# Kernel optimization log

Hardware: AMD Instinct MI355X
Metric: run time of the kernel (lower is better)

Reference implementation:

```python
import jax, jax.numpy as jnp
import numpy as np
import math

B, C, N = 8, 128, 16384
H = 4
DK = C // H
COUT = 128
EPS = 1e-5

def _ln(x, g, b):
    # x: (B,H,N,DK); g,b: (H,DK) -> per-head LayerNorm over last dim
    mu = jnp.mean(x, axis=-1, keepdims=True)
    var = jnp.mean((x - mu) ** 2, axis=-1, keepdims=True)
    xh = (x - mu) / jnp.sqrt(var + EPS)
    return xh * g[None, :, None, :] + b[None, :, None, :]

def setup_inputs() -> dict:
    key = jax.random.key(0)
    ks = jax.random.split(key, 12)
    s = 0.02
    return {
        "x": jax.random.normal(ks[0], (B, C, N), jnp.float32),
        "Wq": jax.random.normal(ks[1], (C, C), jnp.float32) * s + 0.01 * jnp.eye(C),
        "bq": jnp.zeros((C,), jnp.float32),
        "Wk": jax.random.normal(ks[2], (C, C), jnp.float32) * s + 0.01 * jnp.eye(C),
        "bk": jnp.zeros((C,), jnp.float32),
        "Wv": jax.random.normal(ks[3], (C, C), jnp.float32) * s + 0.01 * jnp.eye(C),
        "bv": jnp.zeros((C,), jnp.float32),
        "gK": jnp.ones((H, DK), jnp.float32),
        "bK": jnp.zeros((H, DK), jnp.float32),
        "gV": jnp.ones((H, DK), jnp.float32),
        "bV": jnp.zeros((H, DK), jnp.float32),
        "Wo": jax.random.normal(ks[4], (COUT, C), jnp.float32) * s,
        "bo": jnp.zeros((COUT,), jnp.float32),
    }

def reference(x, Wq, bq, Wk, bk, Wv, bv, gK, bK, gV, bV, Wo, bo):
    # x: (B, C, N) -> (B, N, C)
    xt = jnp.transpose(x, (0, 2, 1))
    def proj(W, b):
        y = xt @ W.T + b                      # (B,N,C)
        return jnp.transpose(y.reshape(B, N, H, DK), (0, 2, 1, 3))  # (B,H,N,DK)
    q = proj(Wq, bq)
    k = proj(Wk, bk)
    v = proj(Wv, bv)
    # galerkin: per-head LayerNorm on K and V (vectorized over heads)
    k = _ln(k, gK, bK)
    v = _ln(v, gV, bV)
    # linear (no-softmax) attention: (Q K^T / sqrt(dk)) / N @ V == Q @ (K^T V) / (sqrt(dk)*N)
    # dropout from F.dropout is treated as identity (deterministic reference)
    kv = jnp.einsum("bhnd,bhne->bhde", k, v)            # (B,H,DK,DK)
    attn = jnp.einsum("bhnd,bhde->bhne", q, kv) / (math.sqrt(DK) * N)
    out = jnp.transpose(attn, (0, 2, 1, 3)).reshape(B, N, C)  # merge heads
    out = out @ Wo.T + bo                                # (B,N,COUT)
    return jnp.transpose(out, (0, 2, 1))                 # (B,COUT,N)
```

## Files before the change

### kernel.cpp

```cpp
#include <hip/hip_runtime.h>
#include <cmath>

#define BB 8
#define CC 128
#define NN 16384
#define HH 4
#define NBK 64
#define SX 272

typedef __attribute__((ext_vector_type(8))) short bf16x8;
typedef __attribute__((ext_vector_type(4))) float f32x4;

#define MFMA(a, b, c) __builtin_amdgcn_mfma_f32_16x16x32_bf16(a, b, c, 0, 0, 0)

__device__ __forceinline__ unsigned short f2b(float f) {
  union { float f; unsigned u; } v; v.f = f;
  unsigned r = v.u + 0x7FFFu + ((v.u >> 16) & 1u);
  return (unsigned short)(r >> 16);
}

__device__ __forceinline__ int xt_addr(int n, int cblk) {
  return n * SX + ((cblk ^ ((n >> 2) & 7)) << 4);
}
__device__ __forceinline__ int kt_byte(int c, int n) {
  return c * 144 + ((((n >> 3) ^ (c & 7)) << 4) | ((n & 7) << 1));
}

__global__ void k_prep(const float* __restrict__ Wq, const float* __restrict__ Wk,
                       const float* __restrict__ Wv, const float* __restrict__ Wo,
                       unsigned short* __restrict__ Wb) {
  const int idx = blockIdx.x * 256 + threadIdx.x;
  const int which = idx >> 14;
  const float* src = (which == 0) ? Wq : (which == 1) ? Wk : (which == 2) ? Wv : Wo;
  Wb[idx] = f2b(src[idx & 16383]);
}

__global__ __launch_bounds__(1024)
void k_xpose(const float* __restrict__ x, unsigned char* __restrict__ xTg) {
  extern __shared__ char lds[];
  const int tid = threadIdx.x;
  const int lane = tid & 63;
  const int w = tid >> 6;
  const int b = blockIdx.y;
  const int n0 = blockIdx.x * 512;

#pragma unroll
  for (int seg = 0; seg < 2; ++seg) {
    const float* xb = x + ((size_t)b * CC + w * 8) * NN + n0 + seg * 256 + lane * 4;
    f32x4 va[8];
#pragma unroll
    for (int cc = 0; cc < 8; ++cc) va[cc] = *(const f32x4*)(xb + (size_t)cc * NN);
#pragma unroll
    for (int j = 0; j < 4; ++j) {
      const int n = seg * 256 + lane * 4 + j;
      bf16x8 pk;
#pragma unroll
      for (int cc = 0; cc < 8; ++cc)
        ((unsigned short*)&pk)[cc] = f2b(va[cc][j]);
      *(bf16x8*)(lds + n * SX + ((w ^ ((n >> 2) & 7)) << 4)) = pk;
    }
  }
  __syncthreads();
  unsigned char* dst = xTg + ((size_t)b * NN + n0) * SX;
  for (int off = tid * 16; off < 512 * SX; off += 16384)
    *(float4*)(dst + off) = *(const float4*)(lds + off);
}

__global__ __launch_bounds__(512, 4)
void k_fuse1(const unsigned char* __restrict__ xTg,
             const unsigned short* __restrict__ Wkb, const unsigned short* __restrict__ Wvb,
             const float* __restrict__ bk, const float* __restrict__ bv,
             const float* __restrict__ gK, const float* __restrict__ bK,
             const float* __restrict__ gV, const float* __restrict__ bV,
             float* __restrict__ kvp) {
  extern __shared__ char lds[];
  char* XT = lds;
  char* KT = lds + 34816;
  char* VT = lds + 53248;
  float* KVS = (float*)lds;

  const int tid = threadIdx.x;
  const int lane = tid & 63;
  const int w = tid >> 6;
  const int b = blockIdx.y;
  const int bx = blockIdx.x;
  const int l15 = lane & 15, l4 = lane >> 4;

  const int ph = w >> 1, pp = w & 1;
  const int kh = w >> 1, khalf = w & 1;

  const unsigned short* Wsrc = pp ? Wvb : Wkb;
  bf16x8 wf[2][4];
#pragma unroll
  for (int mf = 0; mf < 2; ++mf)
#pragma unroll
    for (int ks = 0; ks < 4; ++ks)
      wf[mf][ks] = *(const bf16x8*)(Wsrc + (ph * 32 + mf * 16 + l15) * 128 + ks * 32 + l4 * 8);

  float bias[2][4], gam[2][4], bet[2][4];
  {
    const float* bsrc = pp ? bv : bk;
    const float* gsrc = pp ? gV : gK;
    const float* esrc = pp ? bV : bK;
#pragma unroll
    for (int mf = 0; mf < 2; ++mf)
#pragma unroll
      for (int r = 0; r < 4; ++r) {
        const int cg = ph * 32 + mf * 16 + l4 * 4 + r;
        bias[mf][r] = bsrc[cg]; gam[mf][r] = gsrc[cg]; bet[mf][r] = esrc[cg];
      }
  }

  f32x4 kvacc[2][2];
#pragma unroll
  for (int i = 0; i < 2; ++i)
#pragma unroll
    for (int j = 0; j < 2; ++j) kvacc[i][j] = (f32x4){0.f, 0.f, 0.f, 0.f};

  for (int ot = 0; ot < 2; ++ot) {
    const int n0 = (bx * 2 + ot) * 128;

    {
      const unsigned char* src = xTg + ((size_t)b * NN + n0) * SX;
      for (int off = tid * 16; off < 128 * SX; off += 8192)
        *(float4*)(XT + off) = *(const float4*)(src + off);
    }
    __syncthreads();

    for (int t = 0; t < 2; ++t) {
      const int nbase = t * 64;
      char* DST = pp ? VT : KT;
#pragma unroll
      for (int nf = 0; nf < 4; ++nf) {
        const int n = nbase + nf * 16 + l15;
        f32x4 a0 = (f32x4){0.f, 0.f, 0.f, 0.f}, a1 = (f32x4){0.f, 0.f, 0.f, 0.f};
#pragma unroll
        for (int ks = 0; ks < 4; ++ks) {
          const bf16x8 xf = *(const bf16x8*)(XT + xt_addr(n, ks * 4 + l4));
          a0 = MFMA(wf[0][ks], xf, a0);
          a1 = MFMA(wf[1][ks], xf, a1);
        }
#pragma unroll
        for (int r = 0; r < 4; ++r) { a0[r] += bias[0][r]; a1[r] += bias[1][r]; }
        float s = 0.f, ss = 0.f;
#pragma unroll
        for (int r = 0; r < 4; ++r) {
          s += a0[r] + a1[r];
          ss += a0[r] * a0[r] + a1[r] * a1[r];
        }
        s += __shfl_xor(s, 16); ss += __shfl_xor(ss, 16);
        s += __shfl_xor(s, 32); ss += __shfl_xor(ss, 32);
        const float mu = s * (1.f / 32.f);
        const float var = ss * (1.f / 32.f) - mu * mu;
        const float rstd = rsqrtf(var + 1e-5f);
        const int nloc = nf * 16 + l15;
#pragma unroll
        for (int r = 0; r < 4; ++r) {
          const int c0k = ph * 32 + l4 * 4 + r;
          *(unsigned short*)(DST + kt_byte(c0k, nloc)) =
              f2b((a0[r] - mu) * rstd * gam[0][r] + bet[0][r]);
          const int c1k = ph * 32 + 16 + l4 * 4 + r;
          *(unsigned short*)(DST + kt_byte(c1k, nloc)) =
              f2b((a1[r] - mu) * rstd * gam[1][r] + bet[1][r]);
        }
      }
      __syncthreads();

#pragma unroll
      for (int mf = 0; mf < 2; ++mf) {
        const int ck = kh * 32 + mf * 16 + l15;
        const bf16x8 ka = *(const bf16x8*)(KT + ck * 144 + (((khalf * 4 + l4) ^ (ck & 7)) << 4));
#pragma unroll
        for (int ef = 0; ef < 2; ++ef) {
          const int cv = kh * 32 + ef * 16 + l15;
          const bf16x8 vb = *(const bf16x8*)(VT + cv * 144 + (((khalf * 4 + l4) ^ (cv & 7)) << 4));
          kvacc[mf][ef] = MFMA(ka, vb, kvacc[mf][ef]);
        }
      }
      __syncthreads();
    }
  }

#pragma unroll
  for (int mf = 0; mf < 2; ++mf)
#pragma unroll
    for (int ef = 0; ef < 2; ++ef)
#pragma unroll
      for (int r = 0; r < 4; ++r) {
        const int d = mf * 16 + l4 * 4 + r, e = ef * 16 + l15;
        KVS[w * 1024 + d * 32 + e] = kvacc[mf][ef][r];
      }
  __syncthreads();
  {
    float* og = kvp + ((size_t)(b * NBK + bx)) * 4096;
#pragma unroll
    for (int i = 0; i < 2; ++i) {
      const int off = i * 2048 + tid * 4;
      const int h = off >> 10, q = off & 1023;
      const f32x4 v0 = *(const f32x4*)(KVS + (2 * h) * 1024 + q);
      const f32x4 v1 = *(const f32x4*)(KVS + (2 * h + 1) * 1024 + q);
      *(f32x4*)(og + off) = v0 + v1;
    }
  }
}

__global__ void k_reduceA(const float* __restrict__ kvp, float* __restrict__ p2) {
  const int blk = blockIdx.x;
  const int s = blk & 7, h = (blk >> 3) & 3, b = blk >> 5;
  const int t = threadIdx.x;
  f32x4 acc = (f32x4){0.f, 0.f, 0.f, 0.f};
  for (int i = 0; i < 8; ++i) {
    const int bx = s * 8 + i;
    acc += *(const f32x4*)(kvp + ((size_t)(b * NBK + bx)) * 4096 + h * 1024 + t * 4);
  }
  *(f32x4*)(p2 + (size_t)blk * 1024 + t * 4) = acc;
}

__global__ void k_reduceB(const float* __restrict__ p2, unsigned short* __restrict__ kvT,
                          const float scale) {
  const int bh = blockIdx.x;
  const int t = threadIdx.x;
  f32x4 acc = (f32x4){0.f, 0.f, 0.f, 0.f};
  for (int s = 0; s < 8; ++s)
    acc += *(const f32x4*)(p2 + ((size_t)bh * 8 + s) * 1024 + t * 4);
#pragma unroll
  for (int j = 0; j < 4; ++j) {
    const int i = t * 4 + j;
    const int d = i >> 5, e = i & 31;
    kvT[(size_t)bh * 1024 + e * 32 + d] = f2b(acc[j] * scale);
  }
}

__global__ __launch_bounds__(512, 4)
void k_pass2(const unsigned char* __restrict__ xTg,
             const unsigned short* __restrict__ Wqb, const float* __restrict__ bq,
             const unsigned short* __restrict__ kvT,
             const unsigned short* __restrict__ Wob, const float* __restrict__ bo,
             float* __restrict__ out) {
  extern __shared__ char lds[];
  char* QS = lds + 34816;
  char* AS = lds + 51200;

  const int tid = threadIdx.x;
  const int lane = tid & 63;
  const int w = tid >> 6;
  const int b = blockIdx.y;
  const int l15 = lane & 15, l4 = lane >> 4;
  const int h = w >> 1, half = w & 1;

  bf16x8 kvf[2];
#pragma unroll
  for (int mf = 0; mf < 2; ++mf)
    kvf[mf] = *(const bf16x8*)(kvT + (((size_t)b * HH + h) * 32 + mf * 16 + l15) * 32 + l4 * 8);
  bf16x8 wq[4], wo[4];
#pragma unroll
  for (int ks = 0; ks < 4; ++ks) {
    wq[ks] = *(const bf16x8*)(Wqb + (w * 16 + l15) * 128 + ks * 32 + l4 * 8);
    wo[ks] = *(const bf16x8*)(Wob + (w * 16 + l15) * 128 + ks * 32 + l4 * 8);
  }
  float bq_r[4], bo_r[4];
#pragma unroll
  for (int r = 0; r < 4; ++r) {
    bq_r[r] = bq[w * 16 + l4 * 4 + r];
    bo_r[r] = bo[w * 16 + l4 * 4 + r];
  }

  float* ob = out + (size_t)b * CC * NN;

  for (int it = 0; it < 4; ++it) {
    const int n0 = blockIdx.x * 256 + it * 64;
    char* XT = (it & 1) ? (lds + 17408) : lds;

    {
      const unsigned char* src = xTg + ((size_t)b * NN + n0) * SX;
      for (int off = tid * 16; off < 64 * SX; off += 8192)
        *(float4*)(XT + off) = *(const float4*)(src + off);
    }
    __syncthreads();

    f32x4 qa[4];
#pragma unroll
    for (int nf = 0; nf < 4; ++nf) qa[nf] = (f32x4){0.f, 0.f, 0.f, 0.f};
#pragma unroll
    for (int ks = 0; ks < 4; ++ks)
#pragma unroll
      for (int nf = 0; nf < 4; ++nf) {
        const int n = nf * 16 + l15;
        const bf16x8 xf = *(const bf16x8*)(XT + xt_addr(n, ks * 4 + l4));
        qa[nf] = MFMA(wq[ks], xf, qa[nf]);
      }
#pragma unroll
    for (int nf = 0; nf < 4; ++nf) {
      const int n = nf * 16 + l15;
      const int c0 = w * 16 + l4 * 4;
      unsigned long long pk = 0;
#pragma unroll
      for (int r = 0; r < 4; ++r)
        pk |= (unsigned long long)f2b(qa[nf][r] + bq_r[r]) << (16 * r);
      *(unsigned long long*)(QS + n * 256 + (((c0 >> 3) ^ (n & 15)) << 4) + ((c0 & 7) << 1)) = pk;
    }
    __syncthreads();

    f32x4 aa[2][2];
#pragma unroll
    for (int i = 0; i < 2; ++i)
#pragma unroll
      for (int j = 0; j < 2; ++j) aa[i][j] = (f32x4){0.f, 0.f, 0.f, 0.f};
    bf16x8 qf[2];
#pragma unroll
    for (int nf = 0; nf < 2; ++nf) {
      const int n = half * 32 + nf * 16 + l15;
      const int cq = h * 32 + l4 * 8;
      qf[nf] = *(const bf16x8*)(QS + n * 256 + ((((cq >> 3)) ^ (n & 15)) << 4));
    }
#pragma unroll
    for (int mf = 0; mf < 2; ++mf)
#pragma unroll
      for (int nf = 0; nf < 2; ++nf) aa[mf][nf] = MFMA(kvf[mf], qf[nf], aa[mf][nf]);
#pragma unroll
    for (int mf = 0; mf < 2; ++mf)
#pragma unroll
      for (int nf = 0; nf < 2; ++nf) {
        const int n = half * 32 + nf * 16 + l15;
        const int e0 = h * 32 + mf * 16 + l4 * 4;
        unsigned long long pk = 0;
#pragma unroll
        for (int r = 0; r < 4; ++r)
          pk |= (unsigned long long)f2b(aa[mf][nf][r]) << (16 * r);
        *(unsigned long long*)(AS + n * 256 + (((e0 >> 3) ^ (n & 15)) << 4) + ((e0 & 7) << 1)) = pk;
      }
    __syncthreads();

    f32x4 oa[4];
#pragma unroll
    for (int nf = 0; nf < 4; ++nf) oa[nf] = (f32x4){0.f, 0.f, 0.f, 0.f};
#pragma unroll
    for (int ks = 0; ks < 4; ++ks)
#pragma unroll
      for (int nf = 0; nf < 4; ++nf) {
        const int n = nf * 16 + l15;
        const bf16x8 af = *(const bf16x8*)(AS + n * 256 + (((ks * 4 + l4) ^ (n & 15)) << 4));
        oa[nf] = MFMA(wo[ks], af, oa[nf]);
      }
#pragma unroll
    for (int nf = 0; nf < 4; ++nf)
#pragma unroll
      for (int r = 0; r < 4; ++r) {
        const int c = w * 16 + l4 * 4 + r;
        ob[(size_t)c * NN + n0 + nf * 16 + l15] = oa[nf][r] + bo_r[r];
      }
  }
}

extern "C" void kernel_launch(void* const* d_in, const int* in_sizes, int n_in,
                              void* d_out, int out_size, void* d_ws, size_t ws_size,
                              hipStream_t stream) {
  const float* x  = (const float*)d_in[0];
  const float* Wq = (const float*)d_in[1];
  const float* bq = (const float*)d_in[2];
  const float* Wk = (const float*)d_in[3];
  const float* bk = (const float*)d_in[4];
  const float* Wv = (const float*)d_in[5];
  const float* bv = (const float*)d_in[6];
  const float* gK = (const float*)d_in[7];
  const float* bK = (const float*)d_in[8];
  const float* gV = (const float*)d_in[9];
  const float* bV = (const float*)d_in[10];
  const float* Wo = (const float*)d_in[11];
  const float* bo = (const float*)d_in[12];
  float* out = (float*)d_out;

  char* ws = (char*)d_ws;
  float* kvp = (float*)ws;
  float* p2  = kvp + (size_t)BB * NBK * 4096;
  unsigned short* kvTb = (unsigned short*)(p2 + 256 * 1024);
  unsigned short* Wb = kvTb + (size_t)BB * HH * 1024;
  unsigned char* xT = (unsigned char*)(Wb + 65536);
  const unsigned short* Wqb = Wb;
  const unsigned short* Wkb = Wb + 16384;
  const unsigned short* Wvb = Wb + 32768;
  const unsigned short* Wob = Wb + 49152;

  (void)hipFuncSetAttribute(reinterpret_cast<const void*>(k_xpose),
                            hipFuncAttributeMaxDynamicSharedMemorySize, 139264);
  (void)hipFuncSetAttribute(reinterpret_cast<const void*>(k_fuse1),
                            hipFuncAttributeMaxDynamicSharedMemorySize, 71680);
  (void)hipFuncSetAttribute(reinterpret_cast<const void*>(k_pass2),
                            hipFuncAttributeMaxDynamicSharedMemorySize, 67584);

  k_prep<<<256, 256, 0, stream>>>(Wq, Wk, Wv, Wo, Wb);

  k_xpose<<<dim3(NN / 512, BB), 1024, 139264, stream>>>(x, xT);

  k_fuse1<<<dim3(NBK, BB), 512, 71680, stream>>>(
      xT, Wkb, Wvb, bk, bv, gK, bK, gV, bV, kvp);

  k_reduceA<<<256, 256, 0, stream>>>(kvp, p2);

  const float scale = 1.0f / (5.65685424949238f * 16384.0f);
  k_reduceB<<<32, 256, 0, stream>>>(p2, kvTb, scale);

  k_pass2<<<dim3(NBK, BB), 512, 67584, stream>>>(
      xT, Wqb, bq, kvTb, Wob, bo, out);
}
```

Measured before the change: 81.51 us.

## Store bf16 x in MFMA fragment layout and read operands directly from global

The transpose kernel now writes x as bf16 in a channel-block-major fragment layout, so each lane's 8-element MFMA operand is one contiguous 16-byte global load. The fuse1 and pass2 kernels drop their LDS staging of x tiles and the barriers around it, load fragments straight from global memory, use much less LDS, and launch twice as many blocks with fewer tokens each. The reduction loop is widened to match the larger number of partials. In exchange, x fragment reads go through global memory or cache without LDS reuse, and more partial KV sums must be written and reduced.

```diff
diff --git a/kernel.cpp b/kernel.cpp
--- a/kernel.cpp
+++ b/kernel.cpp
@@ -5,8 +5,8 @@
 #define CC 128
 #define NN 16384
 #define HH 4
-#define NBK 64
-#define SX 272
+#define NC1 128
+#define NC2 128
 
 typedef __attribute__((ext_vector_type(8))) short bf16x8;
 typedef __attribute__((ext_vector_type(4))) float f32x4;
@@ -19,9 +19,6 @@
   return (unsigned short)(r >> 16);
 }
 
-__device__ __forceinline__ int xt_addr(int n, int cblk) {
-  return n * SX + ((cblk ^ ((n >> 2) & 7)) << 4);
-}
 __device__ __forceinline__ int kt_byte(int c, int n) {
   return c * 144 + ((((n >> 3) ^ (c & 7)) << 4) | ((n & 7) << 1));
 }
@@ -36,47 +33,51 @@
 }
 
 __global__ __launch_bounds__(1024)
-void k_xpose(const float* __restrict__ x, unsigned char* __restrict__ xTg) {
+void k_xpose(const float* __restrict__ x, unsigned short* __restrict__ xF) {
   extern __shared__ char lds[];
+  float* XS = (float*)lds;
   const int tid = threadIdx.x;
   const int lane = tid & 63;
   const int w = tid >> 6;
   const int b = blockIdx.y;
   const int n0 = blockIdx.x * 512;
 
-#pragma unroll
-  for (int seg = 0; seg < 2; ++seg) {
-    const float* xb = x + ((size_t)b * CC + w * 8) * NN + n0 + seg * 256 + lane * 4;
-    f32x4 va[8];
-#pragma unroll
-    for (int cc = 0; cc < 8; ++cc) va[cc] = *(const f32x4*)(xb + (size_t)cc * NN);
-#pragma unroll
-    for (int j = 0; j < 4; ++j) {
-      const int n = seg * 256 + lane * 4 + j;
+  for (int g = 0; g < 2; ++g) {
+    if (g) __syncthreads();
+#pragma unroll
+    for (int r = 0; r < 4; ++r) {
+      const int cl = w * 4 + r;
+      const float* src = x + ((size_t)b * CC + g * 64 + cl) * NN + n0;
+      const float4 v0 = *(const float4*)(src + lane * 4);
+      const float4 v1 = *(const float4*)(src + 256 + lane * 4);
+      *(float4*)(XS + cl * 512 + lane * 4) = v0;
+      *(float4*)(XS + cl * 512 + 256 + lane * 4) = v1;
+    }
+    __syncthreads();
+    const int n = tid & 511;
+    const int cblk2 = tid >> 9;
+#pragma unroll
+    for (int cb = 0; cb < 4; ++cb) {
+      const int cbl = cb * 2 + cblk2;
       bf16x8 pk;
 #pragma unroll
       for (int cc = 0; cc < 8; ++cc)
-        ((unsigned short*)&pk)[cc] = f2b(va[cc][j]);
-      *(bf16x8*)(lds + n * SX + ((w ^ ((n >> 2) & 7)) << 4)) = pk;
-    }
-  }
-  __syncthreads();
-  unsigned char* dst = xTg + ((size_t)b * NN + n0) * SX;
-  for (int off = tid * 16; off < 512 * SX; off += 16384)
-    *(float4*)(dst + off) = *(const float4*)(lds + off);
+        ((unsigned short*)&pk)[cc] = f2b(XS[(cbl * 8 + cc) * 512 + n]);
+      *(bf16x8*)(xF + (((size_t)b * 16 + g * 8 + cbl) * NN + n0 + n) * 8) = pk;
+    }
+  }
 }
 
 __global__ __launch_bounds__(512, 4)
-void k_fuse1(const unsigned char* __restrict__ xTg,
+void k_fuse1(const unsigned short* __restrict__ xF,
              const unsigned short* __restrict__ Wkb, const unsigned short* __restrict__ Wvb,
              const float* __restrict__ bk, const float* __restrict__ bv,
              const float* __restrict__ gK, const float* __restrict__ bK,
              const float* __restrict__ gV, const float* __restrict__ bV,
              float* __restrict__ kvp) {
   extern __shared__ char lds[];
-  char* XT = lds;
-  char* KT = lds + 34816;
-  char* VT = lds + 53248;
+  char* KT = lds;
+  char* VT = lds + 18432;
   float* KVS = (float*)lds;
 
   const int tid = threadIdx.x;
@@ -117,68 +118,59 @@
 #pragma unroll
     for (int j = 0; j < 2; ++j) kvacc[i][j] = (f32x4){0.f, 0.f, 0.f, 0.f};
 
-  for (int ot = 0; ot < 2; ++ot) {
-    const int n0 = (bx * 2 + ot) * 128;
-
-    {
-      const unsigned char* src = xTg + ((size_t)b * NN + n0) * SX;
-      for (int off = tid * 16; off < 128 * SX; off += 8192)
-        *(float4*)(XT + off) = *(const float4*)(src + off);
-    }
-    __syncthreads();
-
-    for (int t = 0; t < 2; ++t) {
-      const int nbase = t * 64;
-      char* DST = pp ? VT : KT;
-#pragma unroll
-      for (int nf = 0; nf < 4; ++nf) {
-        const int n = nbase + nf * 16 + l15;
-        f32x4 a0 = (f32x4){0.f, 0.f, 0.f, 0.f}, a1 = (f32x4){0.f, 0.f, 0.f, 0.f};
-#pragma unroll
-        for (int ks = 0; ks < 4; ++ks) {
-          const bf16x8 xf = *(const bf16x8*)(XT + xt_addr(n, ks * 4 + l4));
-          a0 = MFMA(wf[0][ks], xf, a0);
-          a1 = MFMA(wf[1][ks], xf, a1);
-        }
-#pragma unroll
-        for (int r = 0; r < 4; ++r) { a0[r] += bias[0][r]; a1[r] += bias[1][r]; }
-        float s = 0.f, ss = 0.f;
-#pragma unroll
-        for (int r = 0; r < 4; ++r) {
-          s += a0[r] + a1[r];
-          ss += a0[r] * a0[r] + a1[r] * a1[r];
-        }
-        s += __shfl_xor(s, 16); ss += __shfl_xor(ss, 16);
-        s += __shfl_xor(s, 32); ss += __shfl_xor(ss, 32);
-        const float mu = s * (1.f / 32.f);
-        const float var = ss * (1.f / 32.f) - mu * mu;
-        const float rstd = rsqrtf(var + 1e-5f);
-        const int nloc = nf * 16 + l15;
-#pragma unroll
-        for (int r = 0; r < 4; ++r) {
-          const int c0k = ph * 32 + l4 * 4 + r;
-          *(unsigned short*)(DST + kt_byte(c0k, nloc)) =
-              f2b((a0[r] - mu) * rstd * gam[0][r] + bet[0][r]);
-          const int c1k = ph * 32 + 16 + l4 * 4 + r;
-          *(unsigned short*)(DST + kt_byte(c1k, nloc)) =
-              f2b((a1[r] - mu) * rstd * gam[1][r] + bet[1][r]);
-        }
-      }
-      __syncthreads();
-
-#pragma unroll
-      for (int mf = 0; mf < 2; ++mf) {
-        const int ck = kh * 32 + mf * 16 + l15;
-        const bf16x8 ka = *(const bf16x8*)(KT + ck * 144 + (((khalf * 4 + l4) ^ (ck & 7)) << 4));
-#pragma unroll
-        for (int ef = 0; ef < 2; ++ef) {
-          const int cv = kh * 32 + ef * 16 + l15;
-          const bf16x8 vb = *(const bf16x8*)(VT + cv * 144 + (((khalf * 4 + l4) ^ (cv & 7)) << 4));
-          kvacc[mf][ef] = MFMA(ka, vb, kvacc[mf][ef]);
-        }
-      }
-      __syncthreads();
-    }
+  const unsigned short* xb = xF + (size_t)b * 16 * NN * 8;
+
+  for (int t = 0; t < 2; ++t) {
+    const int nt = bx * 128 + t * 64;
+    char* DST = pp ? VT : KT;
+#pragma unroll
+    for (int nf = 0; nf < 4; ++nf) {
+      const int n = nt + nf * 16 + l15;
+      f32x4 a0 = (f32x4){0.f, 0.f, 0.f, 0.f}, a1 = (f32x4){0.f, 0.f, 0.f, 0.f};
+#pragma unroll
+      for (int ks = 0; ks < 4; ++ks) {
+        const bf16x8 xf = *(const bf16x8*)(xb + ((size_t)(ks * 4 + l4) * NN + n) * 8);
+        a0 = MFMA(wf[0][ks], xf, a0);
+        a1 = MFMA(wf[1][ks], xf, a1);
+      }
+#pragma unroll
+      for (int r = 0; r < 4; ++r) { a0[r] += bias[0][r]; a1[r] += bias[1][r]; }
+      float s = 0.f, ss = 0.f;
+#pragma unroll
+      for (int r = 0; r < 4; ++r) {
+        s += a0[r] + a1[r];
+        ss += a0[r] * a0[r] + a1[r] * a1[r];
+      }
+      s += __shfl_xor(s, 16); ss += __shfl_xor(ss, 16);
+      s += __shfl_xor(s, 32); ss += __shfl_xor(ss, 32);
+      const float mu = s * (1.f / 32.f);
+      const float var = ss * (1.f / 32.f) - mu * mu;
+      const float rstd = rsqrtf(var + 1e-5f);
+      const int nloc = nf * 16 + l15;
+#pragma unroll
+      for (int r = 0; r < 4; ++r) {
+        const int c0k = ph * 32 + l4 * 4 + r;
+        *(unsigned short*)(DST + kt_byte(c0k, nloc)) =
+            f2b((a0[r] - mu) * rstd * gam[0][r] + bet[0][r]);
+        const int c1k = ph * 32 + 16 + l4 * 4 + r;
+        *(unsigned short*)(DST + kt_byte(c1k, nloc)) =
+            f2b((a1[r] - mu) * rstd * gam[1][r] + bet[1][r]);
+      }
+    }
+    __syncthreads();
+
+#pragma unroll
+    for (int mf = 0; mf < 2; ++mf) {
+      const int ck = kh * 32 + mf * 16 + l15;
+      const bf16x8 ka = *(const bf16x8*)(KT + ck * 144 + (((khalf * 4 + l4) ^ (ck & 7)) << 4));
+#pragma unroll
+      for (int ef = 0; ef < 2; ++ef) {
+        const int cv = kh * 32 + ef * 16 + l15;
+        const bf16x8 vb = *(const bf16x8*)(VT + cv * 144 + (((khalf * 4 + l4) ^ (cv & 7)) << 4));
+        kvacc[mf][ef] = MFMA(ka, vb, kvacc[mf][ef]);
+      }
+    }
+    __syncthreads();
   }
 
 #pragma unroll
@@ -192,7 +184,7 @@
       }
   __syncthreads();
   {
-    float* og = kvp + ((size_t)(b * NBK + bx)) * 4096;
+    float* og = kvp + ((size_t)(b * NC1 + bx)) * 4096;
 #pragma unroll
     for (int i = 0; i < 2; ++i) {
       const int off = i * 2048 + tid * 4;
@@ -209,9 +201,9 @@
   const int s = blk & 7, h = (blk >> 3) & 3, b = blk >> 5;
   const int t = threadIdx.x;
   f32x4 acc = (f32x4){0.f, 0.f, 0.f, 0.f};
-  for (int i = 0; i < 8; ++i) {
-    const int bx = s * 8 + i;
-    acc += *(const f32x4*)(kvp + ((size_t)(b * NBK + bx)) * 4096 + h * 1024 + t * 4);
+  for (int i = 0; i < 16; ++i) {
+    const int bx = s * 16 + i;
+    acc += *(const f32x4*)(kvp + ((size_t)(b * NC1 + bx)) * 4096 + h * 1024 + t * 4);
   }
   *(f32x4*)(p2 + (size_t)blk * 1024 + t * 4) = acc;
 }
@@ -232,14 +224,14 @@
 }
 
 __global__ __launch_bounds__(512, 4)
-void k_pass2(const unsigned char* __restrict__ xTg,
+void k_pass2(const unsigned short* __restrict__ xF,
              const unsigned short* __restrict__ Wqb, const float* __restrict__ bq,
              const unsigned short* __restrict__ kvT,
              const unsigned short* __restrict__ Wob, const float* __restrict__ bo,
              float* __restrict__ out) {
   extern __shared__ char lds[];
-  char* QS = lds + 34816;
-  char* AS = lds + 51200;
+  char* QS = lds;
+  char* AS = lds + 16384;
 
   const int tid = threadIdx.x;
   const int lane = tid & 63;
@@ -265,18 +257,11 @@
     bo_r[r] = bo[w * 16 + l4 * 4 + r];
   }
 
+  const unsigned short* xb = xF + (size_t)b * 16 * NN * 8;
   float* ob = out + (size_t)b * CC * NN;
 
-  for (int it = 0; it < 4; ++it) {
-    const int n0 = blockIdx.x * 256 + it * 64;
-    char* XT = (it & 1) ? (lds + 17408) : lds;
-
-    {
-      const unsigned char* src = xTg + ((size_t)b * NN + n0) * SX;
-      for (int off = tid * 16; off < 64 * SX; off += 8192)
-        *(float4*)(XT + off) = *(const float4*)(src + off);
-    }
-    __syncthreads();
+  for (int it = 0; it < 2; ++it) {
+    const int n0 = blockIdx.x * 128 + it * 64;
 
     f32x4 qa[4];
 #pragma unroll
@@ -285,8 +270,8 @@
     for (int ks = 0; ks < 4; ++ks)
 #pragma unroll
       for (int nf = 0; nf < 4; ++nf) {
-        const int n = nf * 16 + l15;
-        const bf16x8 xf = *(const bf16x8*)(XT + xt_addr(n, ks * 4 + l4));
+        const int n = n0 + nf * 16 + l15;
+        const bf16x8 xf = *(const bf16x8*)(xb + ((size_t)(ks * 4 + l4) * NN + n) * 8);
         qa[nf] = MFMA(wq[ks], xf, qa[nf]);
       }
 #pragma unroll
@@ -372,34 +357,34 @@
 
   char* ws = (char*)d_ws;
   float* kvp = (float*)ws;
-  float* p2  = kvp + (size_t)BB * NBK * 4096;
+  float* p2  = kvp + (size_t)BB * NC1 * 4096;
   unsigned short* kvTb = (unsigned short*)(p2 + 256 * 1024);
   unsigned short* Wb = kvTb + (size_t)BB * HH * 1024;
-  unsigned char* xT = (unsigned char*)(Wb + 65536);
+  unsigned short* xF = Wb + 65536;
   const unsigned short* Wqb = Wb;
   const unsigned short* Wkb = Wb + 16384;
   const unsigned short* Wvb = Wb + 32768;
   const unsigned short* Wob = Wb + 49152;
 
   (void)hipFuncSetAttribute(reinterpret_cast<const void*>(k_xpose),
-                            hipFuncAttributeMaxDynamicSharedMemorySize, 139264);
+                            hipFuncAttributeMaxDynamicSharedMemorySize, 131072);
   (void)hipFuncSetAttribute(reinterpret_cast<const void*>(k_fuse1),
-                            hipFuncAttributeMaxDynamicSharedMemorySize, 71680);
+                            hipFuncAttributeMaxDynamicSharedMemorySize, 36864);
   (void)hipFuncSetAttribute(reinterpret_cast<const void*>(k_pass2),
-                            hipFuncAttributeMaxDynamicSharedMemorySize, 67584);
+                            hipFuncAttributeMaxDynamicSharedMemorySize, 32768);
 
   k_prep<<<256, 256, 0, stream>>>(Wq, Wk, Wv, Wo, Wb);
 
-  k_xpose<<<dim3(NN / 512, BB), 1024, 139264, stream>>>(x, xT);
-
-  k_fuse1<<<dim3(NBK, BB), 512, 71680, stream>>>(
-      xT, Wkb, Wvb, bk, bv, gK, bK, gV, bV, kvp);
+  k_xpose<<<dim3(NN / 512, BB), 1024, 131072, stream>>>(x, xF);
+
+  k_fuse1<<<dim3(NC1, BB), 512, 36864, stream>>>(
+      xF, Wkb, Wvb, bk, bv, gK, bK, gV, bV, kvp);
 
   k_reduceA<<<256, 256, 0, stream>>>(kvp, p2);
 
   const float scale = 1.0f / (5.65685424949238f * 16384.0f);
   k_reduceB<<<32, 256, 0, stream>>>(p2, kvTb, scale);
 
-  k_pass2<<<dim3(NBK, BB), 512, 67584, stream>>>(
-      xT, Wqb, bq, kvTb, Wob, bo, out);
-}
+  k_pass2<<<dim3(NC2, BB), 512, 32768, stream>>>(
+      xF, Wqb, bq, kvTb, Wob, bo, out);
+}
```

Result: slower. 106.5 us (+30.7%).
